# Kernel optimization log

Hardware: AMD Instinct MI355X
Metric: run time of the kernel (lower is better)

The kernel has to match this reference:

```python
import jax, jax.numpy as jnp
import numpy as np

NUM_NODES = 40000
NUM_EDGES = 400000
DIM = 128
NUM_REL = 502  # num_relation * 2
NUM_HEAD = 1


def setup_inputs() -> dict:
    key = jax.random.key(0)
    ks = jax.random.split(key, 16)
    d = DIM
    return {
        "curr_stat": jax.random.normal(ks[0], (NUM_NODES, d), jnp.float32),
        "last_stat": jax.random.normal(ks[1], (NUM_NODES, d), jnp.float32),
        "relemb_weight": jax.random.normal(ks[2], (NUM_REL, d), jnp.float32),
        "selfrel_weight": jax.random.normal(ks[3], (1, d), jnp.float32),
        "Wq": jax.random.normal(ks[4], (2 * d, d), jnp.float32) * (1.0 / np.sqrt(2 * d)),
        "bq": jax.random.normal(ks[5], (d,), jnp.float32) * 0.02,
        "Wk": jax.random.normal(ks[6], (2 * d, d), jnp.float32) * (1.0 / np.sqrt(2 * d)),
        "bk": jax.random.normal(ks[7], (d,), jnp.float32) * 0.02,
        "Wv": jax.random.normal(ks[8], (d, d), jnp.float32) * (1.0 / np.sqrt(d)),
        "bv": jax.random.normal(ks[9], (d,), jnp.float32) * 0.02,
        "dyn_weight": jax.random.normal(ks[10], (d, d), jnp.float32) * (1.0 / np.sqrt(d)),
        "edge_index": jax.random.randint(ks[11], (2, NUM_EDGES), 0, NUM_NODES, jnp.int32),
        "edge_type": jax.random.randint(ks[12], (NUM_EDGES,), 0, NUM_REL, jnp.int32),
    }


def _segment_softmax(scores, seg, num_segments):
    # scores: [E, H]; softmax over edges sharing the same destination segment
    m = jax.ops.segment_max(scores, seg, num_segments=num_segments)  # [N, H]
    e = jnp.exp(scores - m[seg])
    s = jax.ops.segment_sum(e, seg, num_segments=num_segments)  # [N, H]
    return e / s[seg]


def reference(curr_stat, last_stat, relemb_weight, selfrel_weight,
              Wq, bq, Wk, bk, Wv, bv, dyn_weight,
              edge_index, edge_type):
    N, D = curr_stat.shape
    H = NUM_HEAD
    HD = D // H

    # append self-loop edges for every node, with the dedicated self-relation
    loop = jnp.arange(N, dtype=edge_index.dtype)
    src = jnp.concatenate([edge_index[0], loop])  # [E_total]
    dst = jnp.concatenate([edge_index[1], loop])  # [E_total]
    type_emb = jnp.concatenate(
        [relemb_weight[edge_type], jnp.broadcast_to(selfrel_weight, (N, D))], axis=0)

    E = src.shape[0]
    # linear projections (x @ W + b); torch Linear stores W transposed, same math
    q = (jnp.concatenate([curr_stat[dst], type_emb], -1) @ Wq + bq).reshape(E, H, HD)
    k = (jnp.concatenate([last_stat[src], type_emb], -1) @ Wk + bk).reshape(E, H, HD)
    v = (last_stat[src] @ Wv + bv).reshape(E, H, HD)

    attn = jnp.sum(q * k, axis=-1) / np.sqrt(HD).astype(np.float32)  # [E, H]

    dyn_prob = _segment_softmax(attn, dst, N)   # [E, H]
    sta_prob = _segment_softmax(-attn, dst, N)  # [E, H]

    counts = jax.ops.segment_sum(jnp.ones((E,), jnp.float32), dst, num_segments=N)
    denom = jnp.maximum(counts, 1.0)[:, None]  # scatter-mean denominator

    feat_dyn = jax.ops.segment_sum((dyn_prob[..., None] * v).reshape(E, D), dst,
                                   num_segments=N) / denom
    feat_sta = jax.ops.segment_sum((sta_prob[..., None] * v).reshape(E, D), dst,
                                   num_segments=N) / denom

    # stack (feat_sta, feat_dyn @ dyn_weight) -> [2, N, D]
    return jnp.stack([feat_sta, feat_dyn @ dyn_weight])
```

## Files before the change

### kernel.cpp

```cpp
#include <hip/hip_runtime.h>
#include <hip/hip_bf16.h>
#include <math.h>

#define DIMC 128
#define CS2L (0.08838834764831845f * 1.4426950408889634f)

typedef __attribute__((ext_vector_type(8))) short short8;
typedef __attribute__((ext_vector_type(4))) float floatx4;
typedef __attribute__((ext_vector_type(2))) float f32x2;

static __device__ __forceinline__ unsigned pk2(float lo, float hi) {
    __hip_bfloat162 h = __float22bfloat162_rn(make_float2(lo, hi));
    return *(unsigned*)&h;
}
static __device__ __forceinline__ unsigned short f2bf(float x) {
    union { float f; unsigned int u; } v; v.f = x;
    unsigned int r = v.u + 0x7FFFu + ((v.u >> 16) & 1u);
    return (unsigned short)(r >> 16);
}
static __device__ __forceinline__ f32x2 bfp(unsigned int u) {
    union { unsigned int i; float f; } a, b;
    a.i = u << 16; b.i = u & 0xFFFF0000u;
    f32x2 r; r.x = a.f; r.y = b.f; return r;
}

template<int CTRL>
static __device__ __forceinline__ float dpp_add(float x) {
    int y = __builtin_amdgcn_update_dpp(0, __float_as_int(x), CTRL, 0xF, 0xF, true);
    return x + __int_as_float(y);
}
static __device__ __forceinline__ float red16(float p) {
    p = dpp_add<0xB1>(p);
    p = dpp_add<0x4E>(p);
    p = dpp_add<0x141>(p);
    p = dpp_add<0x140>(p);
    return p;
}

struct PrepArgs {
    const float* W[6];
    unsigned short* F[6];
    float wscale[6];
    const float* relemb; const float* selfrel;
    float* TypeEmb;
    int* deg;
    int R; int N;
};

__global__ __launch_bounds__(64) void prep_all(PrepArgs a)
{
    int b = blockIdx.x;
    int lane = threadIdx.x;
    if (b < 192) {
        int mat = b >> 5, ts = b & 31;
        int s = ts & 3, t = ts >> 2;
        int q = lane >> 4, c = lane & 15;
        const float* W = a.W[mat];
        float sc = a.wscale[mat];
        unsigned short o[8];
        #pragma unroll
        for (int j = 0; j < 8; ++j)
            o[j] = f2bf(W[(long)(s * 32 + q * 8 + j) * DIMC + t * 16 + c] * sc);
        uint4 u;
        u.x = (unsigned)o[0] | ((unsigned)o[1] << 16);
        u.y = (unsigned)o[2] | ((unsigned)o[3] << 16);
        u.z = (unsigned)o[4] | ((unsigned)o[5] << 16);
        u.w = (unsigned)o[6] | ((unsigned)o[7] << 16);
        ((uint4*)a.F[mat])[ts * 64 + lane] = u;
    } else if (b < 192 + a.R + 1) {
        int r = b - 192;
        const float* src = (r < a.R) ? (a.relemb + (long)r * DIMC) : a.selfrel;
        float2 v = ((const float2*)src)[lane];
        ((float2*)(a.TypeEmb + (long)r * DIMC))[lane] = v;
    } else {
        int i = (b - (192 + a.R + 1)) * 64 + lane;
        if (i < a.N) a.deg[i] = 0;
    }
}

struct GemmM5 {
    const float*          Af[5];
    const unsigned short* Ab[5];
    const unsigned short* F[5];
    const float*          bias[5];
    float                 bscale[5];
    float*                outf[5];
    unsigned short*       outb[5];
    int                   ostride[5];
    int                   ooff[5];
    int                   M[5];
    const int*            hist_dst;
    int*                  hist_deg;
    int                   hist_E;
};

__global__ __launch_bounds__(256) void gemm_mfma(GemmM5 g)
{
    __shared__ uint4 wlds[2048];

    if (blockIdx.y == 5) {
        int i = blockIdx.x * blockDim.x + threadIdx.x;
        int stride = gridDim.x * blockDim.x;
        for (; i < g.hist_E; i += stride) atomicAdd(&g.hist_deg[g.hist_dst[i]], 1);
        return;
    }

    const int which = blockIdx.y;
    const int M = g.M[which];
    if ((int)blockIdx.x * 64 >= M) return;

    const float*          __restrict__ Af   = g.Af[which];
    const unsigned short* __restrict__ Ab   = g.Ab[which];
    const unsigned short* __restrict__ F    = g.F[which];
    const float*          __restrict__ bias = g.bias[which];
    const float bsc = g.bscale[which];
    float*          __restrict__ outf = g.outf[which];
    unsigned short* __restrict__ outb = g.outb[which];
    const int ostride = g.ostride[which];
    const int ooff    = g.ooff[which];

    const int wave = threadIdx.x >> 6;
    const int lane = threadIdx.x & 63;
    const int q = lane >> 4, c = lane & 15;
    const int rowbase = blockIdx.x * 64 + wave * 16;

    {
        const uint4* Fp = (const uint4*)F;
        #pragma unroll
        for (int j = 0; j < 8; ++j)
            wlds[threadIdx.x + j * 256] = Fp[threadIdx.x + j * 256];
    }

    int rowA = rowbase + c; if (rowA > M - 1) rowA = M - 1;
    short8 af[4];
    if (Af) {
        const float* Ar = Af + (long)rowA * DIMC + q * 8;
        #pragma unroll
        for (int s = 0; s < 4; ++s) {
            float4 x0 = *(const float4*)(Ar + s * 32);
            float4 x1 = *(const float4*)(Ar + s * 32 + 4);
            uint4 u;
            u.x = pk2(x0.x, x0.y);
            u.y = pk2(x0.z, x0.w);
            u.z = pk2(x1.x, x1.y);
            u.w = pk2(x1.z, x1.w);
            af[s] = *(short8*)&u;
        }
    } else {
        const unsigned short* Ar = Ab + (long)rowA * DIMC + q * 8;
        #pragma unroll
        for (int s = 0; s < 4; ++s) {
            uint4 u = *(const uint4*)(Ar + s * 32);
            af[s] = *(short8*)&u;
        }
    }

    floatx4 acc[8];
    #pragma unroll
    for (int t = 0; t < 8; ++t) {
        float b = bias ? bias[t * 16 + c] * bsc : 0.0f;
        acc[t] = (floatx4){b, b, b, b};
    }

    __syncthreads();

    #pragma unroll
    for (int t = 0; t < 8; ++t)
        #pragma unroll
        for (int s = 0; s < 4; ++s) {
            uint4 u = wlds[(t * 4 + s) * 64 + lane];
            acc[t] = __builtin_amdgcn_mfma_f32_16x16x32_bf16(af[s], *(short8*)&u, acc[t], 0, 0, 0);
        }

    if (outf) {
        #pragma unroll
        for (int t = 0; t < 8; ++t)
            #pragma unroll
            for (int r = 0; r < 4; ++r) {
                int row = rowbase + q * 4 + r;
                if (row < M)
                    outf[(long)row * DIMC + t * 16 + c] = acc[t][r];
            }
    } else {
        #pragma unroll
        for (int t = 0; t < 8; ++t)
            #pragma unroll
            for (int r = 0; r < 4; ++r) {
                float other = __shfl_xor(acc[t][r], 1);
                int row = rowbase + q * 4 + r;
                if ((lane & 1) == 0 && row < M) {
                    unsigned word = pk2(acc[t][r], other);
                    ((unsigned*)outb)[((long)row * 64 + t * 8 + (c >> 1))
                                      * (long)ostride + ooff] = word;
                }
            }
    }
}

__global__ __launch_bounds__(256) void partial_sums(const int* __restrict__ deg,
                                                    int* __restrict__ partial, int N)
{
    __shared__ int sh[256];
    int t = threadIdx.x;
    int beg = blockIdx.x * 1024 + t * 4;
    int s = 0;
    if (beg + 3 < N) { int4 v = *(const int4*)(deg + beg); s = v.x + v.y + v.z + v.w; }
    else { for (int j = 0; j < 4; ++j) if (beg + j < N) s += deg[beg + j]; }
    sh[t] = s;
    __syncthreads();
    for (int d = 128; d >= 1; d >>= 1) {
        if (t < d) sh[t] += sh[t + d];
        __syncthreads();
    }
    if (t == 0) partial[blockIdx.x] = sh[0];
}

__global__ __launch_bounds__(256) void scan_write_offsets(const int* __restrict__ deg,
                                                          const int* __restrict__ partial,
                                                          int* __restrict__ offs,
                                                          int* __restrict__ cursor, int N, int nb)
{
    __shared__ int sh[256];
    __shared__ int sbase;
    int t = threadIdx.x;
    if (t < 64) {
        int v = (t < nb && t < (int)blockIdx.x) ? partial[t] : 0;
        #pragma unroll
        for (int d = 32; d >= 1; d >>= 1) v += __shfl_xor(v, d);
        if (t == 0) sbase = v;
    }
    int beg = blockIdx.x * 1024 + t * 4;
    int d0 = 0, d1 = 0, d2 = 0, d3 = 0;
    if (beg + 3 < N) { int4 v = *(const int4*)(deg + beg); d0 = v.x; d1 = v.y; d2 = v.z; d3 = v.w; }
    else {
        if (beg < N)     d0 = deg[beg];
        if (beg + 1 < N) d1 = deg[beg + 1];
        if (beg + 2 < N) d2 = deg[beg + 2];
        if (beg + 3 < N) d3 = deg[beg + 3];
    }
    int s = d0 + d1 + d2 + d3;
    sh[t] = s;
    __syncthreads();
    for (int d = 1; d < 256; d <<= 1) {
        int v = (t >= d) ? sh[t - d] : 0;
        __syncthreads();
        sh[t] += v;
        __syncthreads();
    }
    int base = sbase + sh[t] - s;
    int o0 = base, o1 = o0 + d0, o2 = o1 + d1, o3 = o2 + d2;
    if (beg < N)     { offs[beg]     = o0; cursor[beg]     = o0; }
    if (beg + 1 < N) { offs[beg + 1] = o1; cursor[beg + 1] = o1; }
    if (beg + 2 < N) { offs[beg + 2] = o2; cursor[beg + 2] = o2; }
    if (beg + 3 < N) { offs[beg + 3] = o3; cursor[beg + 3] = o3; }
}

__global__ void scatter_kernel(const int* __restrict__ src, const int* __restrict__ dst,
                               const int* __restrict__ etype, int* __restrict__ cursor,
                               int2* __restrict__ sedge, int E)
{
    int e = blockIdx.x * blockDim.x + threadIdx.x;
    if (e < E) {
        int d = dst[e];
        int p = atomicAdd(&cursor[d], 1);
        sedge[p] = make_int2(src[e] << 8, etype[e] << 9);
    }
}

__global__ __launch_bounds__(256) void node_kernel(
    const float* __restrict__ Qn,
    const char*  __restrict__ Kb,
    const char*  __restrict__ Vb,
    const char*  __restrict__ QKb,
    const int* __restrict__ offs, const int* __restrict__ deg,
    const int2* __restrict__ sedge,
    float* __restrict__ out_sta, uint4* __restrict__ feat_dyn,
    int N, int R)
{
    int n = (blockIdx.x * blockDim.x + threadIdx.x) >> 6;
    int lane = threadIdx.x & 63;
    if (n >= N) return;
    const int ql = lane & 15;
    const int qt = lane >> 4;
    const int lo16 = ql << 4;
    const int lo32 = ql << 5;

    int base = offs[n];
    int dcnt = deg[n];
    int etot = dcnt + 1;

    const float4* qp = (const float4*)(Qn + (long)n * DIMC + ql * 8);
    float4 qa = qp[0], qb = qp[1];
    f32x2 q01; q01.x = qa.x; q01.y = qa.y;
    f32x2 q23; q23.x = qa.z; q23.y = qa.w;
    f32x2 q45; q45.x = qb.x; q45.y = qb.y;
    f32x2 q67; q67.x = qb.z; q67.y = qb.w;

    float s_d = 0.0f, s_s = 0.0f;
    f32x2 accd0 = {0.f, 0.f}, accd1 = accd0, accd2 = accd0, accd3 = accd0;
    f32x2 accs0 = accd0, accs1 = accd0, accs2 = accd0, accs3 = accd0;

    const int selfK = n << 8, selfQ = R << 9;

    int T = (etot + 3) >> 2;
    for (int it = 0; it < T; ++it) {
        int i = 4 * it + qt;
        bool vv = i < etot;
        bool re = i < dcnt;
        int2 e = re ? sedge[base + i] : make_int2(selfK, selfQ);

        uint4 kx  = *(const uint4*)(Kb + e.x + lo16);
        uint4 vx  = *(const uint4*)(Vb + e.x + lo16);
        uint4 qk0 = *(const uint4*)(QKb + e.y + lo32);
        uint4 qk1 = *(const uint4*)(QKb + e.y + lo32 + 16);

        f32x2 a0 = q01 + bfp(qk0.x), a1 = q23 + bfp(qk0.z);
        f32x2 a2 = q45 + bfp(qk1.x), a3 = q67 + bfp(qk1.z);
        f32x2 k0 = bfp(kx.x) + bfp(qk0.y), k1 = bfp(kx.y) + bfp(qk0.w);
        f32x2 k2 = bfp(kx.z) + bfp(qk1.y), k3 = bfp(kx.w) + bfp(qk1.w);
        f32x2 dp = a0 * k0;
        dp += a1 * k1;
        dp += a2 * k2;
        dp += a3 * k3;
        float p = red16(dp.x + dp.y);

        float wd = vv ? exp2f(p)  : 0.0f;
        float ws = vv ? exp2f(-p) : 0.0f;
        s_d += wd; s_s += ws;

        f32x2 v0 = bfp(vx.x), v1 = bfp(vx.y), v2 = bfp(vx.z), v3 = bfp(vx.w);
        accd0 += v0 * wd; accd1 += v1 * wd; accd2 += v2 * wd; accd3 += v3 * wd;
        accs0 += v0 * ws; accs1 += v1 * ws; accs2 += v2 * ws; accs3 += v3 * ws;
    }

    #define MRG(x) { x += __shfl_xor(x, 16); x += __shfl_xor(x, 32); }
    MRG(s_d) MRG(s_s)
    MRG(accd0.x) MRG(accd0.y) MRG(accd1.x) MRG(accd1.y)
    MRG(accd2.x) MRG(accd2.y) MRG(accd3.x) MRG(accd3.y)
    MRG(accs0.x) MRG(accs0.y) MRG(accs1.x) MRG(accs1.y)
    MRG(accs2.x) MRG(accs2.y) MRG(accs3.x) MRG(accs3.y)
    #undef MRG

    if (qt == 0) {
        float denom = (float)(dcnt + 1);
        float id_ = 1.0f / (s_d * denom);
        float is_ = 1.0f / (s_s * denom);
        float4* op = (float4*)(out_sta + (long)n * DIMC + ql * 8);
        op[0] = make_float4(accs0.x * is_, accs0.y * is_, accs1.x * is_, accs1.y * is_);
        op[1] = make_float4(accs2.x * is_, accs2.y * is_, accs3.x * is_, accs3.y * is_);
        uint4 w;
        w.x = pk2(accd0.x * id_, accd0.y * id_);
        w.y = pk2(accd1.x * id_, accd1.y * id_);
        w.z = pk2(accd2.x * id_, accd2.y * id_);
        w.w = pk2(accd3.x * id_, accd3.y * id_);
        feat_dyn[(unsigned)n * 16u + ql] = w;
    }
}

extern "C" void kernel_launch(void* const* d_in, const int* in_sizes, int n_in,
                              void* d_out, int out_size, void* d_ws, size_t ws_size,
                              hipStream_t stream)
{
    const float* curr    = (const float*)d_in[0];
    const float* last    = (const float*)d_in[1];
    const float* relemb  = (const float*)d_in[2];
    const float* selfrel = (const float*)d_in[3];
    const float* Wq      = (const float*)d_in[4];
    const float* bq      = (const float*)d_in[5];
    const float* Wk      = (const float*)d_in[6];
    const float* bk      = (const float*)d_in[7];
    const float* Wv      = (const float*)d_in[8];
    const float* bv      = (const float*)d_in[9];
    const float* dynw    = (const float*)d_in[10];
    const int*   eidx    = (const int*)d_in[11];
    const int*   etype   = (const int*)d_in[12];
    float* out = (float*)d_out;

    const int N = in_sizes[0] / DIMC;
    const int E = in_sizes[12];
    const int R = in_sizes[2] / DIMC;
    const int* esrc = eidx;
    const int* edst = eidx + E;

    char* wp = (char*)d_ws;
    auto alloc = [&](size_t bytes) { char* r = wp; wp += (bytes + 15) & ~(size_t)15; return r; };
    size_t nd = (size_t)N * DIMC;
    float*          Qn    = (float*)alloc(nd * 4);
    unsigned short* Kb    = (unsigned short*)alloc((size_t)N * 256);
    unsigned short* Vb    = (unsigned short*)alloc((size_t)N * 256);
    unsigned short* Fdb   = (unsigned short*)alloc(nd * 2);
    uint4*          QKre  = (uint4*)alloc((size_t)(R + 1) * 32 * 16);
    float*          TypeEmb = (float*)alloc((size_t)(R + 2) * DIMC * 4);
    unsigned short* FW[6];
    for (int m = 0; m < 6; ++m) FW[m] = (unsigned short*)alloc(2048 * 8 * 2);
    int*            deg   = (int*)alloc((size_t)N * 4);
    int*            offs  = (int*)alloc((size_t)N * 4);
    int*            cursor= (int*)alloc((size_t)N * 4);
    int2*           sedge = (int2*)alloc((size_t)E * 8);
    int*            partial = (int*)alloc(256 * 4);

    const int gblk = N / 64;
    const int sblk = (N + 1023) / 1024;

    PrepArgs pa;
    pa.W[0] = Wq;   pa.W[1] = Wk;   pa.W[2] = Wv;
    pa.W[3] = dynw; pa.W[4] = Wq + (size_t)DIMC * DIMC; pa.W[5] = Wk + (size_t)DIMC * DIMC;
    pa.wscale[0] = CS2L; pa.wscale[1] = 1.0f; pa.wscale[2] = 1.0f;
    pa.wscale[3] = 1.0f; pa.wscale[4] = CS2L; pa.wscale[5] = 1.0f;
    for (int m = 0; m < 6; ++m) pa.F[m] = FW[m];
    pa.relemb = relemb; pa.selfrel = selfrel; pa.TypeEmb = TypeEmb;
    pa.deg = deg; pa.R = R; pa.N = N;
    int pgrid = 192 + (R + 1) + (N + 63) / 64;
    hipLaunchKernelGGL(prep_all, dim3(pgrid), dim3(64), 0, stream, pa);

    GemmM5 g5;
    for (int s = 0; s < 5; ++s) { g5.Ab[s] = nullptr; g5.outf[s] = nullptr; g5.outb[s] = nullptr; g5.bscale[s] = 1.0f; }
    g5.Af[0] = curr;    g5.F[0] = FW[0]; g5.bias[0] = nullptr; g5.outf[0] = Qn;
    g5.ostride[0] = 1;  g5.ooff[0] = 0;  g5.M[0] = N;
    g5.Af[1] = last;    g5.F[1] = FW[1]; g5.bias[1] = nullptr; g5.outb[1] = Kb;
    g5.ostride[1] = 1;  g5.ooff[1] = 0;  g5.M[1] = N;
    g5.Af[2] = last;    g5.F[2] = FW[2]; g5.bias[2] = bv;      g5.outb[2] = Vb;
    g5.ostride[2] = 1;  g5.ooff[2] = 0;  g5.M[2] = N;
    g5.Af[3] = TypeEmb; g5.F[3] = FW[4]; g5.bias[3] = bq;      g5.outb[3] = (unsigned short*)QKre;
    g5.ostride[3] = 2;  g5.ooff[3] = 0;  g5.M[3] = R + 1;      g5.bscale[3] = CS2L;
    g5.Af[4] = TypeEmb; g5.F[4] = FW[5]; g5.bias[4] = bk;      g5.outb[4] = (unsigned short*)QKre;
    g5.ostride[4] = 2;  g5.ooff[4] = 1;  g5.M[4] = R + 1;
    g5.hist_dst = edst; g5.hist_deg = deg; g5.hist_E = E;
    hipLaunchKernelGGL(gemm_mfma, dim3(gblk, 6), dim3(256), 0, stream, g5);

    hipLaunchKernelGGL(partial_sums, dim3(sblk), dim3(256), 0, stream, deg, partial, N);
    hipLaunchKernelGGL(scan_write_offsets, dim3(sblk), dim3(256), 0, stream,
                       deg, partial, offs, cursor, N, sblk);
    hipLaunchKernelGGL(scatter_kernel, dim3((E + 255) / 256), dim3(256), 0, stream,
                       esrc, edst, etype, cursor, sedge, E);

    hipLaunchKernelGGL(node_kernel, dim3((N + 3) / 4), dim3(256), 0, stream,
                       Qn, (const char*)Kb, (const char*)Vb, (const char*)QKre,
                       offs, deg, sedge, out, (uint4*)Fdb, N, R);

    GemmM5 gf;
    for (int s = 0; s < 5; ++s) { gf.Af[s] = nullptr; gf.Ab[s] = nullptr; gf.outf[s] = nullptr; gf.outb[s] = nullptr; gf.M[s] = 0; gf.bscale[s] = 1.0f; }
    gf.Ab[0] = Fdb; gf.F[0] = FW[3]; gf.bias[0] = nullptr; gf.outf[0] = out + nd;
    gf.ostride[0] = 1; gf.ooff[0] = 0; gf.M[0] = N;
    gf.hist_dst = edst; gf.hist_deg = deg; gf.hist_E = 0;
    hipLaunchKernelGGL(gemm_mfma, dim3(gblk, 1), dim3(256), 0, stream, gf);
}
```

Before: 218.0 us.

## Fuse K and V projections sharing A tile; store Q as bf16; widen per-edge lanes

The K and V projections of last_stat now run in one block that loads and converts the A rows once and reuses them for both weight matrices, so the grid drops from six y-slices to five. Q is now written as bf16 instead of fp32, halving its footprint and read traffic in the node kernel. The node kernel gives each edge 8 lanes of 16 elements instead of 16 lanes of 8, which cuts the per-edge shuffle reduction and processes 8 edges per iteration. In exchange, bf16 Q adds precision loss and each lane now holds more registers.

```diff
diff --git a/kernel.cpp b/kernel.cpp
--- a/kernel.cpp
+++ b/kernel.cpp
@@ -29,11 +29,10 @@
     int y = __builtin_amdgcn_update_dpp(0, __float_as_int(x), CTRL, 0xF, 0xF, true);
     return x + __int_as_float(y);
 }
-static __device__ __forceinline__ float red16(float p) {
+static __device__ __forceinline__ float red8(float p) {
     p = dpp_add<0xB1>(p);
     p = dpp_add<0x4E>(p);
     p = dpp_add<0x141>(p);
-    p = dpp_add<0x140>(p);
     return p;
 }
 
@@ -89,6 +88,9 @@
     int                   ostride[5];
     int                   ooff[5];
     int                   M[5];
+    const unsigned short* F2;
+    const float*          bias2;
+    unsigned short*       outb2;
     const int*            hist_dst;
     int*                  hist_deg;
     int                   hist_E;
@@ -98,10 +100,93 @@
 {
     __shared__ uint4 wlds[2048];
 
-    if (blockIdx.y == 5) {
+    if (blockIdx.y == 4) {
         int i = blockIdx.x * blockDim.x + threadIdx.x;
         int stride = gridDim.x * blockDim.x;
         for (; i < g.hist_E; i += stride) atomicAdd(&g.hist_deg[g.hist_dst[i]], 1);
+        return;
+    }
+
+    const int wave = threadIdx.x >> 6;
+    const int lane = threadIdx.x & 63;
+    const int q = lane >> 4, c = lane & 15;
+
+    if (blockIdx.y == 1) {
+        const int M = g.M[1];
+        if ((int)blockIdx.x * 64 >= M) return;
+        const int rowbase = blockIdx.x * 64 + wave * 16;
+
+        {
+            const uint4* Fp = (const uint4*)g.F[1];
+            #pragma unroll
+            for (int j = 0; j < 8; ++j)
+                wlds[threadIdx.x + j * 256] = Fp[threadIdx.x + j * 256];
+        }
+        int rowA = rowbase + c; if (rowA > M - 1) rowA = M - 1;
+        short8 af[4];
+        {
+            const float* Ar = g.Af[1] + (long)rowA * DIMC + q * 8;
+            #pragma unroll
+            for (int s = 0; s < 4; ++s) {
+                float4 x0 = *(const float4*)(Ar + s * 32);
+                float4 x1 = *(const float4*)(Ar + s * 32 + 4);
+                uint4 u;
+                u.x = pk2(x0.x, x0.y);
+                u.y = pk2(x0.z, x0.w);
+                u.z = pk2(x1.x, x1.y);
+                u.w = pk2(x1.z, x1.w);
+                af[s] = *(short8*)&u;
+            }
+        }
+        floatx4 acc[8];
+        #pragma unroll
+        for (int t = 0; t < 8; ++t) acc[t] = (floatx4){0.f, 0.f, 0.f, 0.f};
+        __syncthreads();
+        #pragma unroll
+        for (int t = 0; t < 8; ++t)
+            #pragma unroll
+            for (int s = 0; s < 4; ++s) {
+                uint4 u = wlds[(t * 4 + s) * 64 + lane];
+                acc[t] = __builtin_amdgcn_mfma_f32_16x16x32_bf16(af[s], *(short8*)&u, acc[t], 0, 0, 0);
+            }
+        __syncthreads();
+        {
+            const uint4* Fp = (const uint4*)g.F2;
+            #pragma unroll
+            for (int j = 0; j < 8; ++j)
+                wlds[threadIdx.x + j * 256] = Fp[threadIdx.x + j * 256];
+        }
+        #pragma unroll
+        for (int t = 0; t < 8; ++t)
+            #pragma unroll
+            for (int r = 0; r < 4; ++r) {
+                float other = __shfl_xor(acc[t][r], 1);
+                int row = rowbase + q * 4 + r;
+                if ((lane & 1) == 0 && row < M)
+                    ((unsigned*)g.outb[1])[(long)row * 64 + t * 8 + (c >> 1)] = pk2(acc[t][r], other);
+            }
+        #pragma unroll
+        for (int t = 0; t < 8; ++t) {
+            float b = g.bias2[t * 16 + c];
+            acc[t] = (floatx4){b, b, b, b};
+        }
+        __syncthreads();
+        #pragma unroll
+        for (int t = 0; t < 8; ++t)
+            #pragma unroll
+            for (int s = 0; s < 4; ++s) {
+                uint4 u = wlds[(t * 4 + s) * 64 + lane];
+                acc[t] = __builtin_amdgcn_mfma_f32_16x16x32_bf16(af[s], *(short8*)&u, acc[t], 0, 0, 0);
+            }
+        #pragma unroll
+        for (int t = 0; t < 8; ++t)
+            #pragma unroll
+            for (int r = 0; r < 4; ++r) {
+                float other = __shfl_xor(acc[t][r], 1);
+                int row = rowbase + q * 4 + r;
+                if ((lane & 1) == 0 && row < M)
+                    ((unsigned*)g.outb2)[(long)row * 64 + t * 8 + (c >> 1)] = pk2(acc[t][r], other);
+            }
         return;
     }
 
@@ -118,10 +203,6 @@
     unsigned short* __restrict__ outb = g.outb[which];
     const int ostride = g.ostride[which];
     const int ooff    = g.ooff[which];
-
-    const int wave = threadIdx.x >> 6;
-    const int lane = threadIdx.x & 63;
-    const int q = lane >> 4, c = lane & 15;
     const int rowbase = blockIdx.x * 64 + wave * 16;
 
     {
@@ -268,7 +349,7 @@
 }
 
 __global__ __launch_bounds__(256) void node_kernel(
-    const float* __restrict__ Qn,
+    const char*  __restrict__ Qb,
     const char*  __restrict__ Kb,
     const char*  __restrict__ Vb,
     const char*  __restrict__ QKb,
@@ -280,80 +361,100 @@
     int n = (blockIdx.x * blockDim.x + threadIdx.x) >> 6;
     int lane = threadIdx.x & 63;
     if (n >= N) return;
-    const int ql = lane & 15;
-    const int qt = lane >> 4;
-    const int lo16 = ql << 4;
-    const int lo32 = ql << 5;
+    const int el = lane & 7;
+    const int g8 = lane >> 3;
+    const int ko = el << 5;
+    const int qo = el << 6;
 
     int base = offs[n];
     int dcnt = deg[n];
     int etot = dcnt + 1;
 
-    const float4* qp = (const float4*)(Qn + (long)n * DIMC + ql * 8);
-    float4 qa = qp[0], qb = qp[1];
-    f32x2 q01; q01.x = qa.x; q01.y = qa.y;
-    f32x2 q23; q23.x = qa.z; q23.y = qa.w;
-    f32x2 q45; q45.x = qb.x; q45.y = qb.y;
-    f32x2 q67; q67.x = qb.z; q67.y = qb.w;
+    f32x2 qr[8];
+    {
+        const uint4* qp = (const uint4*)(Qb + ((long)n << 8) + ko);
+        uint4 w0 = qp[0], w1 = qp[1];
+        qr[0] = bfp(w0.x); qr[1] = bfp(w0.y); qr[2] = bfp(w0.z); qr[3] = bfp(w0.w);
+        qr[4] = bfp(w1.x); qr[5] = bfp(w1.y); qr[6] = bfp(w1.z); qr[7] = bfp(w1.w);
+    }
 
     float s_d = 0.0f, s_s = 0.0f;
-    f32x2 accd0 = {0.f, 0.f}, accd1 = accd0, accd2 = accd0, accd3 = accd0;
-    f32x2 accs0 = accd0, accs1 = accd0, accs2 = accd0, accs3 = accd0;
+    f32x2 ad[8], as_[8];
+    #pragma unroll
+    for (int j = 0; j < 8; ++j) { ad[j] = (f32x2){0.f, 0.f}; as_[j] = ad[j]; }
 
     const int selfK = n << 8, selfQ = R << 9;
 
-    int T = (etot + 3) >> 2;
+    int T = (etot + 7) >> 3;
     for (int it = 0; it < T; ++it) {
-        int i = 4 * it + qt;
+        int i = 8 * it + g8;
         bool vv = i < etot;
         bool re = i < dcnt;
         int2 e = re ? sedge[base + i] : make_int2(selfK, selfQ);
 
-        uint4 kx  = *(const uint4*)(Kb + e.x + lo16);
-        uint4 vx  = *(const uint4*)(Vb + e.x + lo16);
-        uint4 qk0 = *(const uint4*)(QKb + e.y + lo32);
-        uint4 qk1 = *(const uint4*)(QKb + e.y + lo32 + 16);
-
-        f32x2 a0 = q01 + bfp(qk0.x), a1 = q23 + bfp(qk0.z);
-        f32x2 a2 = q45 + bfp(qk1.x), a3 = q67 + bfp(qk1.z);
-        f32x2 k0 = bfp(kx.x) + bfp(qk0.y), k1 = bfp(kx.y) + bfp(qk0.w);
-        f32x2 k2 = bfp(kx.z) + bfp(qk1.y), k3 = bfp(kx.w) + bfp(qk1.w);
-        f32x2 dp = a0 * k0;
-        dp += a1 * k1;
-        dp += a2 * k2;
-        dp += a3 * k3;
-        float p = red16(dp.x + dp.y);
+        uint4 k0 = *(const uint4*)(Kb + e.x + ko);
+        uint4 k1 = *(const uint4*)(Kb + e.x + ko + 16);
+        uint4 v0 = *(const uint4*)(Vb + e.x + ko);
+        uint4 v1 = *(const uint4*)(Vb + e.x + ko + 16);
+        uint4 qA = *(const uint4*)(QKb + e.y + qo);
+        uint4 qB = *(const uint4*)(QKb + e.y + qo + 16);
+        uint4 qC = *(const uint4*)(QKb + e.y + qo + 32);
+        uint4 qD = *(const uint4*)(QKb + e.y + qo + 48);
+
+        f32x2 dp;
+        dp  = (qr[0] + bfp(qA.x)) * (bfp(k0.x) + bfp(qA.y));
+        dp += (qr[1] + bfp(qA.z)) * (bfp(k0.y) + bfp(qA.w));
+        dp += (qr[2] + bfp(qB.x)) * (bfp(k0.z) + bfp(qB.y));
+        dp += (qr[3] + bfp(qB.z)) * (bfp(k0.w) + bfp(qB.w));
+        dp += (qr[4] + bfp(qC.x)) * (bfp(k1.x) + bfp(qC.y));
+        dp += (qr[5] + bfp(qC.z)) * (bfp(k1.y) + bfp(qC.w));
+        dp += (qr[6] + bfp(qD.x)) * (bfp(k1.z) + bfp(qD.y));
+        dp += (qr[7] + bfp(qD.z)) * (bfp(k1.w) + bfp(qD.w));
+        float p = red8(dp.x + dp.y);
 
         float wd = vv ? exp2f(p)  : 0.0f;
         float ws = vv ? exp2f(-p) : 0.0f;
         s_d += wd; s_s += ws;
 
-        f32x2 v0 = bfp(vx.x), v1 = bfp(vx.y), v2 = bfp(vx.z), v3 = bfp(vx.w);
-        accd0 += v0 * wd; accd1 += v1 * wd; accd2 += v2 * wd; accd3 += v3 * wd;
-        accs0 += v0 * ws; accs1 += v1 * ws; accs2 += v2 * ws; accs3 += v3 * ws;
-    }
-
-    #define MRG(x) { x += __shfl_xor(x, 16); x += __shfl_xor(x, 32); }
+        f32x2 vp[8];
+        vp[0] = bfp(v0.x); vp[1] = bfp(v0.y); vp[2] = bfp(v0.z); vp[3] = bfp(v0.w);
+        vp[4] = bfp(v1.x); vp[5] = bfp(v1.y); vp[6] = bfp(v1.z); vp[7] = bfp(v1.w);
+        #pragma unroll
+        for (int j = 0; j < 8; ++j) {
+            ad[j]  += vp[j] * wd;
+            as_[j] += vp[j] * ws;
+        }
+    }
+
+    #define MRG(x) { x += __shfl_xor(x, 8); x += __shfl_xor(x, 16); x += __shfl_xor(x, 32); }
     MRG(s_d) MRG(s_s)
-    MRG(accd0.x) MRG(accd0.y) MRG(accd1.x) MRG(accd1.y)
-    MRG(accd2.x) MRG(accd2.y) MRG(accd3.x) MRG(accd3.y)
-    MRG(accs0.x) MRG(accs0.y) MRG(accs1.x) MRG(accs1.y)
-    MRG(accs2.x) MRG(accs2.y) MRG(accs3.x) MRG(accs3.y)
+    #pragma unroll
+    for (int j = 0; j < 8; ++j) {
+        MRG(ad[j].x)  MRG(ad[j].y)
+        MRG(as_[j].x) MRG(as_[j].y)
+    }
     #undef MRG
 
-    if (qt == 0) {
+    if (g8 == 0) {
         float denom = (float)(dcnt + 1);
         float id_ = 1.0f / (s_d * denom);
         float is_ = 1.0f / (s_s * denom);
-        float4* op = (float4*)(out_sta + (long)n * DIMC + ql * 8);
-        op[0] = make_float4(accs0.x * is_, accs0.y * is_, accs1.x * is_, accs1.y * is_);
-        op[1] = make_float4(accs2.x * is_, accs2.y * is_, accs3.x * is_, accs3.y * is_);
-        uint4 w;
-        w.x = pk2(accd0.x * id_, accd0.y * id_);
-        w.y = pk2(accd1.x * id_, accd1.y * id_);
-        w.z = pk2(accd2.x * id_, accd2.y * id_);
-        w.w = pk2(accd3.x * id_, accd3.y * id_);
-        feat_dyn[(unsigned)n * 16u + ql] = w;
+        float4* op = (float4*)(out_sta + (long)n * DIMC + el * 16);
+        op[0] = make_float4(as_[0].x * is_, as_[0].y * is_, as_[1].x * is_, as_[1].y * is_);
+        op[1] = make_float4(as_[2].x * is_, as_[2].y * is_, as_[3].x * is_, as_[3].y * is_);
+        op[2] = make_float4(as_[4].x * is_, as_[4].y * is_, as_[5].x * is_, as_[5].y * is_);
+        op[3] = make_float4(as_[6].x * is_, as_[6].y * is_, as_[7].x * is_, as_[7].y * is_);
+        uint4 w0, w1;
+        w0.x = pk2(ad[0].x * id_, ad[0].y * id_);
+        w0.y = pk2(ad[1].x * id_, ad[1].y * id_);
+        w0.z = pk2(ad[2].x * id_, ad[2].y * id_);
+        w0.w = pk2(ad[3].x * id_, ad[3].y * id_);
+        w1.x = pk2(ad[4].x * id_, ad[4].y * id_);
+        w1.y = pk2(ad[5].x * id_, ad[5].y * id_);
+        w1.z = pk2(ad[6].x * id_, ad[6].y * id_);
+        w1.w = pk2(ad[7].x * id_, ad[7].y * id_);
+        feat_dyn[(unsigned)n * 16u + el * 2]     = w0;
+        feat_dyn[(unsigned)n * 16u + el * 2 + 1] = w1;
     }
 }
 
@@ -385,7 +486,7 @@
     char* wp = (char*)d_ws;
     auto alloc = [&](size_t bytes) { char* r = wp; wp += (bytes + 15) & ~(size_t)15; return r; };
     size_t nd = (size_t)N * DIMC;
-    float*          Qn    = (float*)alloc(nd * 4);
+    unsigned short* Qb    = (unsigned short*)alloc((size_t)N * 256);
     unsigned short* Kb    = (unsigned short*)alloc((size_t)N * 256);
     unsigned short* Vb    = (unsigned short*)alloc((size_t)N * 256);
     unsigned short* Fdb   = (unsigned short*)alloc(nd * 2);
@@ -414,19 +515,16 @@
     hipLaunchKernelGGL(prep_all, dim3(pgrid), dim3(64), 0, stream, pa);
 
     GemmM5 g5;
-    for (int s = 0; s < 5; ++s) { g5.Ab[s] = nullptr; g5.outf[s] = nullptr; g5.outb[s] = nullptr; g5.bscale[s] = 1.0f; }
-    g5.Af[0] = curr;    g5.F[0] = FW[0]; g5.bias[0] = nullptr; g5.outf[0] = Qn;
-    g5.ostride[0] = 1;  g5.ooff[0] = 0;  g5.M[0] = N;
-    g5.Af[1] = last;    g5.F[1] = FW[1]; g5.bias[1] = nullptr; g5.outb[1] = Kb;
-    g5.ostride[1] = 1;  g5.ooff[1] = 0;  g5.M[1] = N;
-    g5.Af[2] = last;    g5.F[2] = FW[2]; g5.bias[2] = bv;      g5.outb[2] = Vb;
-    g5.ostride[2] = 1;  g5.ooff[2] = 0;  g5.M[2] = N;
-    g5.Af[3] = TypeEmb; g5.F[3] = FW[4]; g5.bias[3] = bq;      g5.outb[3] = (unsigned short*)QKre;
-    g5.ostride[3] = 2;  g5.ooff[3] = 0;  g5.M[3] = R + 1;      g5.bscale[3] = CS2L;
-    g5.Af[4] = TypeEmb; g5.F[4] = FW[5]; g5.bias[4] = bk;      g5.outb[4] = (unsigned short*)QKre;
-    g5.ostride[4] = 2;  g5.ooff[4] = 1;  g5.M[4] = R + 1;
+    for (int s = 0; s < 5; ++s) { g5.Af[s] = nullptr; g5.Ab[s] = nullptr; g5.outf[s] = nullptr; g5.outb[s] = nullptr; g5.bias[s] = nullptr; g5.bscale[s] = 1.0f; g5.ostride[s] = 1; g5.ooff[s] = 0; g5.M[s] = 0; }
+    g5.Af[0] = curr;    g5.F[0] = FW[0]; g5.outb[0] = Qb;  g5.M[0] = N;
+    g5.Af[1] = last;    g5.F[1] = FW[1]; g5.outb[1] = Kb;  g5.M[1] = N;
+    g5.F2 = FW[2]; g5.bias2 = bv; g5.outb2 = Vb;
+    g5.Af[2] = TypeEmb; g5.F[2] = FW[4]; g5.bias[2] = bq;  g5.outb[2] = (unsigned short*)QKre;
+    g5.ostride[2] = 2;  g5.ooff[2] = 0;  g5.M[2] = R + 1;  g5.bscale[2] = CS2L;
+    g5.Af[3] = TypeEmb; g5.F[3] = FW[5]; g5.bias[3] = bk;  g5.outb[3] = (unsigned short*)QKre;
+    g5.ostride[3] = 2;  g5.ooff[3] = 1;  g5.M[3] = R + 1;
     g5.hist_dst = edst; g5.hist_deg = deg; g5.hist_E = E;
-    hipLaunchKernelGGL(gemm_mfma, dim3(gblk, 6), dim3(256), 0, stream, g5);
+    hipLaunchKernelGGL(gemm_mfma, dim3(gblk, 5), dim3(256), 0, stream, g5);
 
     hipLaunchKernelGGL(partial_sums, dim3(sblk), dim3(256), 0, stream, deg, partial, N);
     hipLaunchKernelGGL(scan_write_offsets, dim3(sblk), dim3(256), 0, stream,
@@ -435,13 +533,13 @@
                        esrc, edst, etype, cursor, sedge, E);
 
     hipLaunchKernelGGL(node_kernel, dim3((N + 3) / 4), dim3(256), 0, stream,
-                       Qn, (const char*)Kb, (const char*)Vb, (const char*)QKre,
+                       (const char*)Qb, (const char*)Kb, (const char*)Vb, (const char*)QKre,
                        offs, deg, sedge, out, (uint4*)Fdb, N, R);
 
     GemmM5 gf;
-    for (int s = 0; s < 5; ++s) { gf.Af[s] = nullptr; gf.Ab[s] = nullptr; gf.outf[s] = nullptr; gf.outb[s] = nullptr; gf.M[s] = 0; gf.bscale[s] = 1.0f; }
-    gf.Ab[0] = Fdb; gf.F[0] = FW[3]; gf.bias[0] = nullptr; gf.outf[0] = out + nd;
-    gf.ostride[0] = 1; gf.ooff[0] = 0; gf.M[0] = N;
+    for (int s = 0; s < 5; ++s) { gf.Af[s] = nullptr; gf.Ab[s] = nullptr; gf.outf[s] = nullptr; gf.outb[s] = nullptr; gf.bias[s] = nullptr; gf.bscale[s] = 1.0f; gf.ostride[s] = 1; gf.ooff[s] = 0; gf.M[s] = 0; }
+    gf.Ab[0] = Fdb; gf.F[0] = FW[3]; gf.outf[0] = out + nd; gf.M[0] = N;
+    gf.F2 = FW[2]; gf.bias2 = bv; gf.outb2 = Vb;
     gf.hist_dst = edst; gf.hist_deg = deg; gf.hist_E = 0;
     hipLaunchKernelGGL(gemm_mfma, dim3(gblk, 1), dim3(256), 0, stream, gf);
 }
```

Measured after the change: 248.7 us. +14.1%, slower.
